# Kernel optimization log

Measured on AMD Instinct MI355X. Metric: run time of the kernel, lower is better.

Reference implementation:

```python
import jax, jax.numpy as jnp
import numpy as np

N_DT, N_OD = 30000, 10000
D_DT, D_OD = 128, 64
H, O = 128, 64
E1, E2, EL = 500000, 300000, 200000


def _w(k, shape):
    return jax.random.normal(k, shape, jnp.float32) / np.sqrt(shape[0]).astype(np.float32)


def setup_inputs() -> dict:
    key = jax.random.key(0)
    ks = jax.random.split(key, 32)
    inp = {
        "x_dt": jax.random.normal(ks[0], (N_DT, D_DT), jnp.float32),
        "x_od": jax.random.normal(ks[1], (N_OD, D_OD), jnp.float32),
        "ei_dt": jax.random.randint(ks[2], (2, E1), 0, N_DT),
        "ei_rev_src": jax.random.randint(ks[3], (E2,), 0, N_DT),
        "ei_rev_dst": jax.random.randint(ks[4], (E2,), 0, N_OD),
        "el_src": jax.random.randint(ks[5], (EL,), 0, N_OD),
        "el_dst": jax.random.randint(ks[6], (EL,), 0, N_DT),
        # ODEncoderModel params
        "od1_wl": _w(ks[7], (D_DT, H)), "od1_wr": _w(ks[8], (D_DT, H)), "od1_b": jnp.zeros((H,), jnp.float32),
        "od2_wl": _w(ks[9], (H, H)),    "od2_wr": _w(ks[10], (D_OD, H)), "od2_b": jnp.zeros((H,), jnp.float32),
        "od3_wl": _w(ks[11], (H, H)),   "od3_wr": _w(ks[12], (H, H)),    "od3_b": jnp.zeros((H,), jnp.float32),
        "od_lw": _w(ks[13], (H, O)),    "od_lb": jnp.zeros((O,), jnp.float32),
        # DetectorTimeEncoder params
        "dt1_wl": _w(ks[14], (D_DT, H)), "dt1_wr": _w(ks[15], (D_DT, H)), "dt1_b": jnp.zeros((H,), jnp.float32),
        "dt2_wl": _w(ks[16], (H, H)),    "dt2_wr": _w(ks[17], (H, H)),    "dt2_b": jnp.zeros((H,), jnp.float32),
        "dt_lw": _w(ks[18], (H, O)),     "dt_lb": jnp.zeros((O,), jnp.float32),
        # EdgeDecoder params (hidden = out_channels = O)
        "dec_w1": _w(ks[19], (2 * O, O)), "dec_b1": jnp.zeros((O,), jnp.float32),
        "dec_w2": _w(ks[20], (O, 1)),     "dec_b2": jnp.zeros((1,), jnp.float32),
    }
    return inp


def sage(x_src, x_dst, row, col, wl, wr, b, n_dst):
    """PyG SAGEConv (aggr='mean', root_weight=True): lin_l(mean_j x_src[j]) + lin_r(x_dst)."""
    msg = jax.ops.segment_sum(x_src[row], col, num_segments=n_dst)  # [n_dst, d_src]
    cnt = jax.ops.segment_sum(jnp.ones_like(col, dtype=x_src.dtype), col, num_segments=n_dst)
    agg = msg / jnp.maximum(cnt, 1.0)[:, None]
    return agg @ wl + x_dst @ wr + b


def reference(x_dt, x_od, ei_dt, ei_rev_src, ei_rev_dst, el_src, el_dst,
              od1_wl, od1_wr, od1_b, od2_wl, od2_wr, od2_b, od3_wl, od3_wr, od3_b, od_lw, od_lb,
              dt1_wl, dt1_wr, dt1_b, dt2_wl, dt2_wr, dt2_b, dt_lw, dt_lb,
              dec_w1, dec_b1, dec_w2, dec_b2):
    r1, c1 = ei_dt[0], ei_dt[1]
    relu = jax.nn.relu
    # OD encoder: dt metapath conv, then two bipartite convs dt->od
    h = relu(sage(x_dt, x_dt, r1, c1, od1_wl, od1_wr, od1_b, N_DT))
    od = relu(sage(h, x_od, ei_rev_src, ei_rev_dst, od2_wl, od2_wr, od2_b, N_OD))
    od = relu(sage(h, od, ei_rev_src, ei_rev_dst, od3_wl, od3_wr, od3_b, N_OD))
    z_od = od @ od_lw + od_lb  # [N_OD, O]
    # DetectorTime encoder: two homogeneous convs on dt graph
    d = relu(sage(x_dt, x_dt, r1, c1, dt1_wl, dt1_wr, dt1_b, N_DT))
    d = relu(sage(d, d, r1, c1, dt2_wl, dt2_wr, dt2_b, N_DT))
    z_dt = d @ dt_lw + dt_lb  # [N_DT, O]
    # Edge decoder: gather pairs, MLP, sigmoid
    z = jnp.concatenate([z_od[el_src], z_dt[el_dst]], axis=-1)  # [EL, 2O]
    z = relu(z @ dec_w1 + dec_b1)
    return jax.nn.sigmoid(z @ dec_w2 + dec_b2).reshape(-1)  # [EL]
```

## Files before the change

### kernel.cpp

```cpp
#include <hip/hip_runtime.h>
#include <hip/hip_bf16.h>

#define NDT 30000
#define NOD 10000
#define NE1 500000
#define NE2 300000
#define NEL 200000
#define CAP_DT 64
#define CAP_OD 96

typedef unsigned short ushort_t;
typedef unsigned int uint_t;
typedef __attribute__((ext_vector_type(8))) short short8;
typedef __attribute__((ext_vector_type(4))) float f32x4;

static constexpr size_t F_BFUSE = 0;
static constexpr size_t F_ENDF  = 64;
static constexpr size_t U_XDT    = 0;
static constexpr size_t U_XOD    = U_XDT + (size_t)NDT * 128;
static constexpr size_t U_AGGX   = U_XOD + (size_t)NOD * 64;
static constexpr size_t U_H      = U_AGGX + (size_t)NDT * 128;
static constexpr size_t U_D1     = U_H + (size_t)NDT * 128;
static constexpr size_t U_AGGH   = U_D1 + (size_t)NDT * 128;
static constexpr size_t U_OD2    = U_AGGH + (size_t)NOD * 128;
static constexpr size_t U_OD3    = U_OD2 + (size_t)NOD * 128;
static constexpr size_t U_WT1A   = U_OD3 + (size_t)NOD * 128;
static constexpr size_t U_WT1B   = U_WT1A + 32768;
static constexpr size_t U_WTOD2  = U_WT1B + 32768;
static constexpr size_t U_WTOD3  = U_WTOD2 + 24576;
static constexpr size_t U_WTDT2  = U_WTOD3 + 32768;
static constexpr size_t U_WLODT  = U_WTDT2 + 32768;
static constexpr size_t U_WLDTT  = U_WLODT + 8192;
static constexpr size_t U_POD    = U_WLDTT + 8192;
static constexpr size_t U_PDT    = U_POD + (size_t)NOD * 64;
static constexpr size_t U_SRC_DT = U_PDT + (size_t)NDT * 64;
static constexpr size_t U_SRC_OD = U_SRC_DT + (size_t)NDT * CAP_DT;
static constexpr size_t U_END    = U_SRC_OD + (size_t)NOD * CAP_OD;
static constexpr size_t I_CNT_DT = 0;
static constexpr size_t I_CNT_OD = 30000;

__device__ __forceinline__ ushort_t f2bf(float f) {
    uint_t u = __float_as_uint(f);
    return (ushort_t)((u + 0x7fffu + ((u >> 16) & 1u)) >> 16);
}
__device__ __forceinline__ float bf2f(uint_t lo16) { return __uint_as_float(lo16 << 16); }

__global__ __launch_bounds__(256) void conv_bf(const float* __restrict__ x_dt, const float* __restrict__ x_od,
                                               ushort_t* __restrict__ xdt_bf, ushort_t* __restrict__ xod_bf) {
    int i = blockIdx.x * 256 + threadIdx.x;
    size_t i4 = (size_t)i * 4;
    const size_t n_dt = (size_t)NDT * 128, n_od = (size_t)NOD * 64;
    if (i4 < n_dt) {
        float4 v = *(const float4*)(x_dt + i4);
        ushort4 o = { f2bf(v.x), f2bf(v.y), f2bf(v.z), f2bf(v.w) };
        *(ushort4*)(xdt_bf + i4) = o;
    } else if (i4 - n_dt < n_od) {
        size_t j = i4 - n_dt;
        float4 v = *(const float4*)(x_od + j);
        ushort4 o = { f2bf(v.x), f2bf(v.y), f2bf(v.z), f2bf(v.w) };
        *(ushort4*)(xod_bf + j) = o;
    }
}

__global__ __launch_bounds__(256) void prep_wt(const float* od1_wl, const float* od1_wr,
                                               const float* dt1_wl, const float* dt1_wr,
                                               const float* od2_wl, const float* od2_wr,
                                               const float* od3_wl, const float* od3_wr,
                                               const float* dt2_wl, const float* dt2_wr,
                                               ushort_t* wt1a, ushort_t* wt1b, ushort_t* wtod2,
                                               ushort_t* wtod3, ushort_t* wtdt2) {
    int i = blockIdx.x * 256 + threadIdx.x;
    const float* wl; const float* wr; ushort_t* dst; int q, KT;
    if (i < 32768)       { q = i;          KT = 256; wl = od1_wl; wr = od1_wr; dst = wt1a; }
    else if (i < 65536)  { q = i - 32768;  KT = 256; wl = dt1_wl; wr = dt1_wr; dst = wt1b; }
    else if (i < 90112)  { q = i - 65536;  KT = 192; wl = od2_wl; wr = od2_wr; dst = wtod2; }
    else if (i < 122880) { q = i - 90112;  KT = 256; wl = od3_wl; wr = od3_wr; dst = wtod3; }
    else if (i < 155648) { q = i - 122880; KT = 256; wl = dt2_wl; wr = dt2_wr; dst = wtdt2; }
    else return;
    int n = q / KT, k = q - n * KT;
    float v = (k < 128) ? wl[(size_t)k * 128 + n] : wr[(size_t)(k - 128) * 128 + n];
    dst[q] = f2bf(v);
}

__global__ __launch_bounds__(256) void fill_direct(const int* __restrict__ r1, const int* __restrict__ c1,
                                                   const int* __restrict__ rev_src, const int* __restrict__ rev_dst,
                                                   int* cnt_dt, ushort_t* srcs_dt,
                                                   int* cnt_od, ushort_t* srcs_od) {
    int b = (blockIdx.x * 256 + threadIdx.x) * 4;
    if (b + 3 < NE1) {
        int4 d = *(const int4*)(c1 + b);
        int4 s = *(const int4*)(r1 + b);
        int p0 = atomicAdd(&cnt_dt[d.x], 1);
        int p1 = atomicAdd(&cnt_dt[d.y], 1);
        int p2 = atomicAdd(&cnt_dt[d.z], 1);
        int p3 = atomicAdd(&cnt_dt[d.w], 1);
        if (p0 < CAP_DT) srcs_dt[d.x * CAP_DT + p0] = (ushort_t)s.x;
        if (p1 < CAP_DT) srcs_dt[d.y * CAP_DT + p1] = (ushort_t)s.y;
        if (p2 < CAP_DT) srcs_dt[d.z * CAP_DT + p2] = (ushort_t)s.z;
        if (p3 < CAP_DT) srcs_dt[d.w * CAP_DT + p3] = (ushort_t)s.w;
    } else {
        for (int i = b; i < NE1; i++) {
            int p = atomicAdd(&cnt_dt[c1[i]], 1);
            if (p < CAP_DT) srcs_dt[c1[i] * CAP_DT + p] = (ushort_t)r1[i];
        }
    }
    if (b + 3 < NE2) {
        int4 d = *(const int4*)(rev_dst + b);
        int4 s = *(const int4*)(rev_src + b);
        int p0 = atomicAdd(&cnt_od[d.x], 1);
        int p1 = atomicAdd(&cnt_od[d.y], 1);
        int p2 = atomicAdd(&cnt_od[d.z], 1);
        int p3 = atomicAdd(&cnt_od[d.w], 1);
        if (p0 < CAP_OD) srcs_od[d.x * CAP_OD + p0] = (ushort_t)s.x;
        if (p1 < CAP_OD) srcs_od[d.y * CAP_OD + p1] = (ushort_t)s.y;
        if (p2 < CAP_OD) srcs_od[d.z * CAP_OD + p2] = (ushort_t)s.z;
        if (p3 < CAP_OD) srcs_od[d.w * CAP_OD + p3] = (ushort_t)s.w;
    } else if (b < NE2) {
        for (int i = b; i < NE2; i++) {
            int p = atomicAdd(&cnt_od[rev_dst[i]], 1);
            if (p < CAP_OD) srcs_od[rev_dst[i] * CAP_OD + p] = (ushort_t)rev_src[i];
        }
    }
}

__global__ __launch_bounds__(64) void seg_mean_bf(const ushort_t* __restrict__ X,
                                                  const int* __restrict__ cnt,
                                                  const ushort_t* __restrict__ srcs, int cap,
                                                  ushort_t* __restrict__ out) {
    int b = blockIdx.x;
    int t = threadIdx.x;
    int deg = cnt[b];
    int n = deg < cap ? deg : cap;
    int start = b * cap;
    float a0 = 0.f, a1 = 0.f, b0 = 0.f, b1 = 0.f, c0 = 0.f, c1 = 0.f, d0 = 0.f, d1 = 0.f;
    int j = 0;
    for (; j + 3 < n; j += 4) {
        int s0 = srcs[start + j], s1 = srcs[start + j + 1];
        int s2 = srcs[start + j + 2], s3 = srcs[start + j + 3];
        uint_t v0 = *(const uint_t*)&X[(size_t)s0 * 128 + 2 * t];
        uint_t v1 = *(const uint_t*)&X[(size_t)s1 * 128 + 2 * t];
        uint_t v2 = *(const uint_t*)&X[(size_t)s2 * 128 + 2 * t];
        uint_t v3 = *(const uint_t*)&X[(size_t)s3 * 128 + 2 * t];
        a0 += bf2f(v0 & 0xffff); a1 += __uint_as_float(v0 & 0xffff0000u);
        b0 += bf2f(v1 & 0xffff); b1 += __uint_as_float(v1 & 0xffff0000u);
        c0 += bf2f(v2 & 0xffff); c1 += __uint_as_float(v2 & 0xffff0000u);
        d0 += bf2f(v3 & 0xffff); d1 += __uint_as_float(v3 & 0xffff0000u);
    }
    for (; j < n; j++) {
        uint_t v = *(const uint_t*)&X[(size_t)srcs[start + j] * 128 + 2 * t];
        a0 += bf2f(v & 0xffff); a1 += __uint_as_float(v & 0xffff0000u);
    }
    float inv = deg > 0 ? 1.f / (float)deg : 0.f;
    float s0 = ((a0 + b0) + (c0 + d0)) * inv;
    float s1 = ((a1 + b1) + (c1 + d1)) * inv;
    *(uint_t*)&out[(size_t)b * 128 + 2 * t] = (uint_t)f2bf(s0) | ((uint_t)f2bf(s1) << 16);
}

template <bool DUAL>
__global__ __launch_bounds__(256) void sage_mfma(
    const ushort_t* __restrict__ A1, int K1,
    const ushort_t* __restrict__ A2, int K2,
    const ushort_t* __restrict__ Wta, const ushort_t* __restrict__ Wtb,
    const float* __restrict__ ba, const float* __restrict__ bb,
    ushort_t* __restrict__ outa, ushort_t* __restrict__ outb, int M) {
    __shared__ __align__(16) ushort_t As[32 * 264];
    __shared__ __align__(16) ushort_t Wsa[128 * 40];
    __shared__ __align__(16) ushort_t Wsb[DUAL ? 128 * 40 : 8];
    const int KT = K1 + K2;
    const int AST = KT + 8;
    int t = threadIdx.x;
    int lane = t & 63, wave = t >> 6;
    int quad = lane >> 4, l16 = lane & 15;
    int mtile = wave & 1, nquad = wave >> 1;
    int mb = blockIdx.x * 32;

    int c1n = 32 * (K1 >> 3);
    for (int c = t; c < c1n; c += 256) {
        int row = c / (K1 >> 3), k8 = (c % (K1 >> 3)) * 8;
        int m = mb + row; if (m >= M) m = M - 1;
        *(short8*)&As[row * AST + k8] = *(const short8*)&A1[(size_t)m * K1 + k8];
    }
    int c2n = 32 * (K2 >> 3);
    for (int c = t; c < c2n; c += 256) {
        int row = c / (K2 >> 3), k8 = (c % (K2 >> 3)) * 8;
        int m = mb + row; if (m >= M) m = M - 1;
        *(short8*)&As[row * AST + K1 + k8] = *(const short8*)&A2[(size_t)m * K2 + k8];
    }

    f32x4 acca[4] = {};
    f32x4 accb[4] = {};
    for (int kc = 0; kc < KT; kc += 32) {
        __syncthreads();
        for (int c = t; c < 512; c += 256) {
            int n = c >> 2, k8 = (c & 3) * 8;
            *(short8*)&Wsa[n * 40 + k8] = *(const short8*)&Wta[(size_t)n * KT + kc + k8];
            if (DUAL)
                *(short8*)&Wsb[n * 40 + k8] = *(const short8*)&Wtb[(size_t)n * KT + kc + k8];
        }
        __syncthreads();
        short8 af = *(const short8*)&As[(mtile * 16 + l16) * AST + kc + quad * 8];
#pragma unroll
        for (int nt = 0; nt < 4; nt++) {
            int n = (nquad * 4 + nt) * 16 + l16;
            short8 bfr = *(const short8*)&Wsa[n * 40 + quad * 8];
            acca[nt] = __builtin_amdgcn_mfma_f32_16x16x32_bf16(af, bfr, acca[nt], 0, 0, 0);
            if (DUAL) {
                short8 bfr2 = *(const short8*)&Wsb[n * 40 + quad * 8];
                accb[nt] = __builtin_amdgcn_mfma_f32_16x16x32_bf16(af, bfr2, accb[nt], 0, 0, 0);
            }
        }
    }
    int mrow = mb + mtile * 16 + quad * 4;
#pragma unroll
    for (int nt = 0; nt < 4; nt++) {
        int n = (nquad * 4 + nt) * 16 + l16;
        float bva = ba[n];
        float bvb = DUAL ? bb[n] : 0.f;
#pragma unroll
        for (int r = 0; r < 4; r++) {
            int m = mrow + r;
            if (m < M) {
                outa[(size_t)m * 128 + n] = f2bf(fmaxf(acca[nt][r] + bva, 0.f));
                if (DUAL) outb[(size_t)m * 128 + n] = f2bf(fmaxf(accb[nt][r] + bvb, 0.f));
            }
        }
    }
}

__global__ __launch_bounds__(256) void lin_mfma(const ushort_t* __restrict__ A,
                                                const ushort_t* __restrict__ Wt,
                                                ushort_t* __restrict__ out, int M) {
    __shared__ __align__(16) ushort_t As[64 * 136];
    __shared__ __align__(16) ushort_t Ws[64 * 40];
    int t = threadIdx.x;
    int lane = t & 63, wave = t >> 6;
    int quad = lane >> 4, l16 = lane & 15;
    int mb = blockIdx.x * 64;
    for (int c = t; c < 1024; c += 256) {
        int row = c >> 4, k8 = (c & 15) * 8;
        int m = mb + row; if (m >= M) m = M - 1;
        *(short8*)&As[row * 136 + k8] = *(const short8*)&A[(size_t)m * 128 + k8];
    }
    f32x4 acc[4] = {};
    for (int kc = 0; kc < 128; kc += 32) {
        __syncthreads();
        for (int c = t; c < 256; c += 256) {
            int n = c >> 2, k8 = (c & 3) * 8;
            *(short8*)&Ws[n * 40 + k8] = *(const short8*)&Wt[(size_t)n * 128 + kc + k8];
        }
        __syncthreads();
        short8 af = *(const short8*)&As[(wave * 16 + l16) * 136 + kc + quad * 8];
#pragma unroll
        for (int nt = 0; nt < 4; nt++) {
            short8 bfr = *(const short8*)&Ws[(nt * 16 + l16) * 40 + quad * 8];
            acc[nt] = __builtin_amdgcn_mfma_f32_16x16x32_bf16(af, bfr, acc[nt], 0, 0, 0);
        }
    }
    int mrow = mb + wave * 16 + quad * 4;
#pragma unroll
    for (int nt = 0; nt < 4; nt++) {
        int n = nt * 16 + l16;
#pragma unroll
        for (int r = 0; r < 4; r++) {
            int m = mrow + r;
            if (m < M) out[(size_t)m * 64 + n] = f2bf(acc[nt][r]);
        }
    }
}

__global__ __launch_bounds__(256) void fuse_dec(const float* __restrict__ od_lw, const float* __restrict__ od_lb,
                                                const float* __restrict__ dt_lw, const float* __restrict__ dt_lb,
                                                const float* __restrict__ w1, const float* __restrict__ b1,
                                                ushort_t* wodt, ushort_t* wdtt, float* bfuse) {
    int i = blockIdx.x * 256 + threadIdx.x;
    if (i < 8192) {
        int r = i >> 6, p = i & 63;
        float s = 0.f;
        for (int j = 0; j < 64; j++) s = fmaf(od_lw[r * 64 + j], w1[j * 64 + p], s);
        wodt[p * 128 + r] = f2bf(s);
    } else if (i < 16384) {
        int q = i - 8192, r = q >> 6, p = q & 63;
        float s = 0.f;
        for (int j = 0; j < 64; j++) s = fmaf(dt_lw[r * 64 + j], w1[(64 + j) * 64 + p], s);
        wdtt[p * 128 + r] = f2bf(s);
    } else if (i < 16448) {
        int p = i - 16384;
        float s = b1[p];
        for (int j = 0; j < 64; j++) {
            s = fmaf(od_lb[j], w1[j * 64 + p], s);
            s = fmaf(dt_lb[j], w1[(64 + j) * 64 + p], s);
        }
        bfuse[p] = s;
    }
}

__global__ __launch_bounds__(256) void decode(const ushort_t* __restrict__ P_od, const ushort_t* __restrict__ P_dt,
                                              const int* __restrict__ el_src, const int* __restrict__ el_dst,
                                              const float* __restrict__ bfuse, const float* __restrict__ w2,
                                              const float* __restrict__ b2v, float* __restrict__ out) {
    __shared__ __align__(16) float bf[64];
    __shared__ __align__(16) float w2s[64];
    int t = threadIdx.x;
    if (t < 64) { bf[t] = bfuse[t]; w2s[t] = w2[t]; }
    __syncthreads();
    int e = blockIdx.x * 256 + t;
    if (e >= NEL) return;
    const uint4* po = (const uint4*)(P_od + (size_t)el_src[e] * 64);
    const uint4* pt = (const uint4*)(P_dt + (size_t)el_dst[e] * 64);
    float acc = 0.f;
#pragma unroll
    for (int c = 0; c < 8; c++) {
        uint4 a = po[c], b = pt[c];
        const uint_t* au = (const uint_t*)&a;
        const uint_t* bu = (const uint_t*)&b;
#pragma unroll
        for (int j = 0; j < 4; j++) {
            int idx = c * 8 + j * 2;
            float lo = bf2f(au[j] & 0xffff) + bf2f(bu[j] & 0xffff) + bf[idx];
            float hi = __uint_as_float(au[j] & 0xffff0000u) + __uint_as_float(bu[j] & 0xffff0000u) + bf[idx + 1];
            acc = fmaf(fmaxf(lo, 0.f), w2s[idx], acc);
            acc = fmaf(fmaxf(hi, 0.f), w2s[idx + 1], acc);
        }
    }
    float z = acc + b2v[0];
    out[e] = 1.f / (1.f + __expf(-z));
}

extern "C" void kernel_launch(void* const* d_in, const int* in_sizes, int n_in,
                              void* d_out, int out_size, void* d_ws, size_t ws_size,
                              hipStream_t stream) {
    float* W = (float*)d_ws;
    ushort_t* U = (ushort_t*)(W + F_ENDF);
    int* I = (int*)(U + U_END);

    const float* x_dt   = (const float*)d_in[0];
    const float* x_od   = (const float*)d_in[1];
    const int* ei       = (const int*)d_in[2];
    const int* r1 = ei;
    const int* c1 = ei + NE1;
    const int* rev_src  = (const int*)d_in[3];
    const int* rev_dst  = (const int*)d_in[4];
    const int* el_src   = (const int*)d_in[5];
    const int* el_dst   = (const int*)d_in[6];
    const float* od1_wl = (const float*)d_in[7],  *od1_wr = (const float*)d_in[8],  *od1_b = (const float*)d_in[9];
    const float* od2_wl = (const float*)d_in[10], *od2_wr = (const float*)d_in[11], *od2_b = (const float*)d_in[12];
    const float* od3_wl = (const float*)d_in[13], *od3_wr = (const float*)d_in[14], *od3_b = (const float*)d_in[15];
    const float* od_lw  = (const float*)d_in[16], *od_lb  = (const float*)d_in[17];
    const float* dt1_wl = (const float*)d_in[18], *dt1_wr = (const float*)d_in[19], *dt1_b = (const float*)d_in[20];
    const float* dt2_wl = (const float*)d_in[21], *dt2_wr = (const float*)d_in[22], *dt2_b = (const float*)d_in[23];
    const float* dt_lw  = (const float*)d_in[24], *dt_lb  = (const float*)d_in[25];
    const float* dec_w1 = (const float*)d_in[26], *dec_b1 = (const float*)d_in[27];
    const float* dec_w2 = (const float*)d_in[28], *dec_b2 = (const float*)d_in[29];

    hipMemsetAsync(I + I_CNT_DT, 0, (NDT + NOD) * sizeof(int), stream);

    conv_bf<<<((NDT * 128 + NOD * 64) / 4 + 255) / 256, 256, 0, stream>>>(x_dt, x_od, U + U_XDT, U + U_XOD);
    prep_wt<<<(155648 + 255) / 256, 256, 0, stream>>>(od1_wl, od1_wr, dt1_wl, dt1_wr, od2_wl, od2_wr,
                                                      od3_wl, od3_wr, dt2_wl, dt2_wr,
                                                      U + U_WT1A, U + U_WT1B, U + U_WTOD2, U + U_WTOD3, U + U_WTDT2);
    fill_direct<<<(NE1 / 4 + 255) / 256, 256, 0, stream>>>(r1, c1, rev_src, rev_dst,
                                                           I + I_CNT_DT, U + U_SRC_DT,
                                                           I + I_CNT_OD, U + U_SRC_OD);
    fuse_dec<<<(16448 + 255) / 256, 256, 0, stream>>>(od_lw, od_lb, dt_lw, dt_lb, dec_w1, dec_b1,
                                                      U + U_WLODT, U + U_WLDTT, W + F_BFUSE);

    seg_mean_bf<<<NDT, 64, 0, stream>>>(U + U_XDT, I + I_CNT_DT, U + U_SRC_DT, CAP_DT, U + U_AGGX);
    sage_mfma<true><<<(NDT + 31) / 32, 256, 0, stream>>>(U + U_AGGX, 128, U + U_XDT, 128,
                                                         U + U_WT1A, U + U_WT1B, od1_b, dt1_b,
                                                         U + U_H, U + U_D1, NDT);
    seg_mean_bf<<<NOD, 64, 0, stream>>>(U + U_H, I + I_CNT_OD, U + U_SRC_OD, CAP_OD, U + U_AGGH);
    sage_mfma<false><<<(NOD + 31) / 32, 256, 0, stream>>>(U + U_AGGH, 128, U + U_XOD, 64,
                                                          U + U_WTOD2, nullptr, od2_b, nullptr,
                                                          U + U_OD2, nullptr, NOD);
    sage_mfma<false><<<(NOD + 31) / 32, 256, 0, stream>>>(U + U_AGGH, 128, U + U_OD2, 128,
                                                          U + U_WTOD3, nullptr, od3_b, nullptr,
                                                          U + U_OD3, nullptr, NOD);
    seg_mean_bf<<<NDT, 64, 0, stream>>>(U + U_D1, I + I_CNT_DT, U + U_SRC_DT, CAP_DT, U + U_AGGX);
    sage_mfma<false><<<(NDT + 31) / 32, 256, 0, stream>>>(U + U_AGGX, 128, U + U_D1, 128,
                                                          U + U_WTDT2, nullptr, dt2_b, nullptr,
                                                          U + U_H, nullptr, NDT);
    lin_mfma<<<(NOD + 63) / 64, 256, 0, stream>>>(U + U_OD3, U + U_WLODT, U + U_POD, NOD);
    lin_mfma<<<(NDT + 63) / 64, 256, 0, stream>>>(U + U_H, U + U_WLDTT, U + U_PDT, NDT);
    decode<<<(NEL + 255) / 256, 256, 0, stream>>>(U + U_POD, U + U_PDT, el_src, el_dst,
                                                  W + F_BFUSE, dec_w2, dec_b2, (float*)d_out);
}
```

Measured before the change: 304.7 us.

## Partition CSR fill by destination slice so atomics stay XCD-local

Replaces the flat per-edge fill kernel with a sliced version. Each block takes one edge chunk and one of eight destination ranges, chosen by blockIdx & 7. The likely intent is to keep the counter atomics and slot writes for a destination range on one XCD's L2, reducing cross-die atomic traffic on MI355X. The cost is that every edge index is read eight times, and per-thread loads become scalar strided loads instead of int4, which adds memory traffic.

```diff
diff --git a/kernel.cpp b/kernel.cpp
--- a/kernel.cpp
+++ b/kernel.cpp
@@ -8,6 +8,7 @@
 #define NEL 200000
 #define CAP_DT 64
 #define CAP_OD 96
+#define NCHUNK 60
 
 typedef unsigned short ushort_t;
 typedef unsigned int uint_t;
@@ -82,43 +83,32 @@
     dst[q] = f2bf(v);
 }
 
-__global__ __launch_bounds__(256) void fill_direct(const int* __restrict__ r1, const int* __restrict__ c1,
+__global__ __launch_bounds__(256) void fill_sliced(const int* __restrict__ r1, const int* __restrict__ c1,
                                                    const int* __restrict__ rev_src, const int* __restrict__ rev_dst,
                                                    int* cnt_dt, ushort_t* srcs_dt,
                                                    int* cnt_od, ushort_t* srcs_od) {
-    int b = (blockIdx.x * 256 + threadIdx.x) * 4;
-    if (b + 3 < NE1) {
-        int4 d = *(const int4*)(c1 + b);
-        int4 s = *(const int4*)(r1 + b);
-        int p0 = atomicAdd(&cnt_dt[d.x], 1);
-        int p1 = atomicAdd(&cnt_dt[d.y], 1);
-        int p2 = atomicAdd(&cnt_dt[d.z], 1);
-        int p3 = atomicAdd(&cnt_dt[d.w], 1);
-        if (p0 < CAP_DT) srcs_dt[d.x * CAP_DT + p0] = (ushort_t)s.x;
-        if (p1 < CAP_DT) srcs_dt[d.y * CAP_DT + p1] = (ushort_t)s.y;
-        if (p2 < CAP_DT) srcs_dt[d.z * CAP_DT + p2] = (ushort_t)s.z;
-        if (p3 < CAP_DT) srcs_dt[d.w * CAP_DT + p3] = (ushort_t)s.w;
-    } else {
-        for (int i = b; i < NE1; i++) {
-            int p = atomicAdd(&cnt_dt[c1[i]], 1);
-            if (p < CAP_DT) srcs_dt[c1[i] * CAP_DT + p] = (ushort_t)r1[i];
-        }
-    }
-    if (b + 3 < NE2) {
-        int4 d = *(const int4*)(rev_dst + b);
-        int4 s = *(const int4*)(rev_src + b);
-        int p0 = atomicAdd(&cnt_od[d.x], 1);
-        int p1 = atomicAdd(&cnt_od[d.y], 1);
-        int p2 = atomicAdd(&cnt_od[d.z], 1);
-        int p3 = atomicAdd(&cnt_od[d.w], 1);
-        if (p0 < CAP_OD) srcs_od[d.x * CAP_OD + p0] = (ushort_t)s.x;
-        if (p1 < CAP_OD) srcs_od[d.y * CAP_OD + p1] = (ushort_t)s.y;
-        if (p2 < CAP_OD) srcs_od[d.z * CAP_OD + p2] = (ushort_t)s.z;
-        if (p3 < CAP_OD) srcs_od[d.w * CAP_OD + p3] = (ushort_t)s.w;
-    } else if (b < NE2) {
-        for (int i = b; i < NE2; i++) {
-            int p = atomicAdd(&cnt_od[rev_dst[i]], 1);
-            if (p < CAP_OD) srcs_od[rev_dst[i] * CAP_OD + p] = (ushort_t)rev_src[i];
+    int s = blockIdx.x & 7;
+    int chunk = blockIdx.x >> 3;
+    int dtLo = s * (NDT / 8), dtHi = dtLo + (NDT / 8);
+    int odLo = s * (NOD / 8), odHi = odLo + (NOD / 8);
+    const int CH1 = (NE1 + NCHUNK - 1) / NCHUNK;
+    const int CH2 = (NE2 + NCHUNK - 1) / NCHUNK;
+    int e0 = chunk * CH1;
+    int e1 = e0 + CH1 < NE1 ? e0 + CH1 : NE1;
+    for (int i = e0 + threadIdx.x; i < e1; i += 256) {
+        int d = c1[i];
+        if (d >= dtLo && d < dtHi) {
+            int p = atomicAdd(&cnt_dt[d], 1);
+            if (p < CAP_DT) srcs_dt[d * CAP_DT + p] = (ushort_t)r1[i];
+        }
+    }
+    e0 = chunk * CH2;
+    e1 = e0 + CH2 < NE2 ? e0 + CH2 : NE2;
+    for (int i = e0 + threadIdx.x; i < e1; i += 256) {
+        int d = rev_dst[i];
+        if (d >= odLo && d < odHi) {
+            int p = atomicAdd(&cnt_od[d], 1);
+            if (p < CAP_OD) srcs_od[d * CAP_OD + p] = (ushort_t)rev_src[i];
         }
     }
 }
@@ -358,9 +348,9 @@
     prep_wt<<<(155648 + 255) / 256, 256, 0, stream>>>(od1_wl, od1_wr, dt1_wl, dt1_wr, od2_wl, od2_wr,
                                                       od3_wl, od3_wr, dt2_wl, dt2_wr,
                                                       U + U_WT1A, U + U_WT1B, U + U_WTOD2, U + U_WTOD3, U + U_WTDT2);
-    fill_direct<<<(NE1 / 4 + 255) / 256, 256, 0, stream>>>(r1, c1, rev_src, rev_dst,
-                                                           I + I_CNT_DT, U + U_SRC_DT,
-                                                           I + I_CNT_OD, U + U_SRC_OD);
+    fill_sliced<<<NCHUNK * 8, 256, 0, stream>>>(r1, c1, rev_src, rev_dst,
+                                                I + I_CNT_DT, U + U_SRC_DT,
+                                                I + I_CNT_OD, U + U_SRC_OD);
     fuse_dec<<<(16448 + 255) / 256, 256, 0, stream>>>(od_lw, od_lb, dt_lw, dt_lb, dec_w1, dec_b1,
                                                       U + U_WLODT, U + U_WLDTT, W + F_BFUSE);
 
```

Result: slower. 317.4 us (+4.2%).
